# Kernel tuning notes

Hardware: AMD Instinct MI355X
Metric: run time of the kernel (lower is better)

## Reference

```python
import jax, jax.numpy as jnp
import numpy as np

B, D, OUT = 16384, 128, 32

def setup_inputs() -> dict:
    key = jax.random.key(0)
    kx, kw, kb = jax.random.split(key, 3)
    x = jax.random.normal(kx, (B, D), dtype=jnp.float32)
    # nn.Linear(in=D*(D+1), out=OUT): weight [OUT, D*(D+1)], bias [OUT]
    fan_in = D * (D + 1)
    bound = 1.0 / np.sqrt(fan_in)
    W = jax.random.uniform(kw, (OUT, fan_in), dtype=jnp.float32, minval=-bound, maxval=bound)
    b = jax.random.uniform(kb, (OUT,), dtype=jnp.float32, minval=-bound, maxval=bound)
    return {"x": x, "W": W, "b": b}

def reference(x, W, b):
    Bn, d = x.shape
    ones = jnp.ones((Bn, 1), dtype=x.dtype)
    xe = jnp.concatenate([x, ones], axis=-1)          # [B, d+1]
    # outer product z[b, i, j] = x[b, i] * xe[b, j]; flatten row-major -> [B, d*(d+1)]
    z = (x[:, :, None] * xe[:, None, :]).reshape(Bn, d * (d + 1))
    y = z @ W.T + b                                    # [B, OUT]
    return y
```

## Files before the change

kernel.cpp:

```cpp
#include <hip/hip_runtime.h>

typedef __attribute__((ext_vector_type(8)))  __bf16 bf16x8;
typedef __attribute__((ext_vector_type(16))) float  f32x16;
typedef unsigned int uint32;

#define D_IN  128
#define N_OUT 32
#define K129  129
#define WROW  16512
#define KE    144
#define NT    8
#define XQ_ELEMS (16384 * 128)
#define WQ_ELEMS (32 * 128 * KE)

__host__ __device__ __forceinline__ int permSlot(int s) {
    int q = s >> 3, h = (s >> 2) & 1, j = s & 3;
    return 16 * (q >> 1) + 8 * h + 4 * (q & 1) + j;
}

__global__ void prep(const float* __restrict__ x, const float* __restrict__ W,
                     __bf16* __restrict__ xq, __bf16* __restrict__ Wq) {
    int t = blockIdx.x * 256 + threadIdx.x;
    {
        const float4* s = reinterpret_cast<const float4*>(x) + (size_t)t * 2;
        float4 a = s[0], b = s[1];
        bf16x8 v = { (__bf16)a.x, (__bf16)a.y, (__bf16)a.z, (__bf16)a.w,
                     (__bf16)b.x, (__bf16)b.y, (__bf16)b.z, (__bf16)b.w };
        reinterpret_cast<bf16x8*>(xq)[t] = v;
    }
    for (int e = t; e < WQ_ELEMS; e += 262144) {
        int oi = e / KE, k = e - oi * KE;
        int o = oi >> 7, sg = oi & 127;
        int i = (sg & ~31) + permSlot(sg & 31);
        float v = (k <= D_IN) ? W[o * WROW + i * K129 + k] : 0.f;
        Wq[e] = (__bf16)v;
    }
}

#define STAGE(BUF, T)                                                              \
  do {                                                                             \
    if (PREP) {                                                                    \
      __builtin_amdgcn_global_load_lds(                                            \
        (const __attribute__((address_space(1))) uint32*)                          \
          (xq + ((rbase + (long)(T) * 32 + r0s) * D_IN + c0s * 8)),                \
        (__attribute__((address_space(3))) uint32*)(&tile[BUF][wave * 1024]),      \
        16, 0, 0);                                                                 \
      __builtin_amdgcn_global_load_lds(                                            \
        (const __attribute__((address_space(1))) uint32*)                          \
          (xq + ((rbase + (long)(T) * 32 + r1s) * D_IN + c1s * 8)),                \
        (__attribute__((address_space(3))) uint32*)(&tile[BUF][wave * 1024 + 512]),\
        16, 0, 0);                                                                 \
    } else {                                                                       \
      const float* s0 = x + (rbase + (long)(T) * 32 + r0s) * D_IN + c0s * 8;       \
      const float* s1 = x + (rbase + (long)(T) * 32 + r1s) * D_IN + c1s * 8;       \
      float4 a0 = *(const float4*)s0, a1 = *(const float4*)(s0 + 4);               \
      float4 b0 = *(const float4*)s1, b1 = *(const float4*)(s1 + 4);               \
      bf16x8 v0 = { (__bf16)a0.x,(__bf16)a0.y,(__bf16)a0.z,(__bf16)a0.w,           \
                    (__bf16)a1.x,(__bf16)a1.y,(__bf16)a1.z,(__bf16)a1.w };         \
      bf16x8 v1 = { (__bf16)b0.x,(__bf16)b0.y,(__bf16)b0.z,(__bf16)b0.w,           \
                    (__bf16)b1.x,(__bf16)b1.y,(__bf16)b1.z,(__bf16)b1.w };         \
      *(bf16x8*)&tile[BUF][(size_t)p0 * 8] = v0;                                   \
      *(bf16x8*)&tile[BUF][(size_t)p1 * 8] = v1;                                   \
    }                                                                              \
  } while (0)

#define COMPUTE(BUF, MT)                                                           \
  {                                                                                \
    const char* tb = (const char*)&tile[BUF][0];                                   \
    bf16x8 Bf[8];                                                                  \
    _Pragma("unroll")                                                              \
    for (int ks = 0; ks < 8; ++ks)                                                 \
      Bf[ks] = *reinterpret_cast<const bf16x8*>(tb + laneB[ks]);                   \
    float s = 0.f;                                                                 \
    _Pragma("unroll")                                                              \
    for (int ct = 0; ct < 4; ++ct) {                                               \
      f32x16 a;                                                                    \
      _Pragma("unroll")                                                            \
      for (int r = 0; r < 16; ++r) a[r] = 0.f;                                     \
      _Pragma("unroll")                                                            \
      for (int ks = 0; ks < 8; ++ks)                                               \
        a = __builtin_amdgcn_mfma_f32_32x32x16_bf16(A[ct][ks], Bf[ks], a, 0, 0, 0);\
      a = __builtin_amdgcn_mfma_f32_32x32x16_bf16(A[ct][8], B8c, a, 0, 0, 0);      \
      _Pragma("unroll")                                                            \
      for (int q = 0; q < 4; ++q)                                                  \
        _Pragma("unroll")                                                          \
        for (int j = 0; j < 4; ++j)                                                \
          s += a[q * 4 + j] * (float)Bf[2 * ct + (q >> 1)][4 * (q & 1) + j];       \
    }                                                                              \
    s += __shfl_xor(s, 32);                                                        \
    if (hi == 0)                                                                   \
      out[(rbase + (long)(MT) * 32 + b32) * N_OUT + o] = s + bias_o;               \
  }

template<int PREP>
__global__ __launch_bounds__(256, 2) void quad5(
    const float* __restrict__ x, const float* __restrict__ W,
    const __bf16* __restrict__ xq, const __bf16* __restrict__ Wq,
    const float* __restrict__ bias, float* __restrict__ out)
{
    __shared__ __align__(16) __bf16 tile[2][32 * 128];

    const int tid  = threadIdx.x;
    const int lane = tid & 63;
    const int wave = tid >> 6;
    const int b32  = lane & 31, hi = lane >> 5;

    const int bid = blockIdx.x;
    const int xcd = bid & 7, idx = bid >> 3;
    const int run = xcd * 8 + (idx & 7);
    const int og  = idx >> 3;
    const int o   = og * 4 + wave;
    const long rbase = (long)run * (NT * 32);
    const float bias_o = bias[o];

    bf16x8 A[4][9];
    #pragma unroll
    for (int ct = 0; ct < 4; ++ct) {
        if (PREP) {
            const __bf16* base = Wq + ((size_t)o * 128 + ct * 32 + b32) * KE + hi * 8;
            #pragma unroll
            for (int ks = 0; ks < 9; ++ks)
                A[ct][ks] = *reinterpret_cast<const bf16x8*>(base + ks * 16);
        } else {
            const int i = ct * 32 + permSlot(b32);
            const float* wr = W + (size_t)o * WROW + (size_t)i * K129;
            #pragma unroll
            for (int ks = 0; ks < 8; ++ks) {
                bf16x8 f;
                #pragma unroll
                for (int r = 0; r < 8; ++r) f[r] = (__bf16)wr[ks * 16 + hi * 8 + r];
                A[ct][ks] = f;
            }
            bf16x8 f;
            #pragma unroll
            for (int r = 0; r < 8; ++r) f[r] = (__bf16)0.f;
            if (hi == 0) f[0] = (__bf16)wr[128];
            A[ct][8] = f;
        }
    }

    bf16x8 B8c;
    #pragma unroll
    for (int r = 0; r < 8; ++r) B8c[r] = (__bf16)0.f;
    if (hi == 0) B8c[0] = (__bf16)1.0f;

    const int p0 = wave * 128 + lane;
    const int r0s = p0 >> 4, c0s = (p0 & 15) ^ (r0s & 15);
    const int p1 = p0 + 64;
    const int r1s = p1 >> 4, c1s = (p1 & 15) ^ (r1s & 15);

    const int rm = b32 & 15;
    int laneB[8];
    #pragma unroll
    for (int ks = 0; ks < 8; ++ks)
        laneB[ks] = b32 * 256 + (((ks * 2 + hi) ^ rm) << 4);

    STAGE(0, 0);
    __syncthreads();

    #pragma unroll
    for (int t2 = 0; t2 < NT / 2; ++t2) {
        if (t2 * 2 + 1 < NT) STAGE(1, t2 * 2 + 1);
        COMPUTE(0, t2 * 2);
        __syncthreads();
        if (t2 * 2 + 2 < NT) STAGE(0, t2 * 2 + 2);
        COMPUTE(1, t2 * 2 + 1);
        __syncthreads();
    }
}

extern "C" void kernel_launch(void* const* d_in, const int* in_sizes, int n_in,
                              void* d_out, int out_size, void* d_ws, size_t ws_size,
                              hipStream_t stream) {
    const float* x    = (const float*)d_in[0];
    const float* W    = (const float*)d_in[1];
    const float* bias = (const float*)d_in[2];
    float* out = (float*)d_out;

    const size_t need = (size_t)(XQ_ELEMS + WQ_ELEMS) * sizeof(__bf16);
    if (ws_size >= need) {
        __bf16* xq = (__bf16*)d_ws;
        __bf16* Wq = xq + XQ_ELEMS;
        prep<<<1024, 256, 0, stream>>>(x, W, xq, Wq);
        quad5<1><<<512, 256, 0, stream>>>(x, W, xq, Wq, bias, out);
    } else {
        quad5<0><<<512, 256, 0, stream>>>(x, W, (const __bf16*)nullptr,
                                          (const __bf16*)nullptr, bias, out);
    }
}
```

Baseline: 27.79 us.

## Deepen x-tile pipeline to four LDS buffers with vmcnt waits and deferred stores

Replaces the double-buffered LDS tile loop with a four-buffer ring that prefetches three tiles ahead. Each step waits only on the outstanding global-to-LDS loads it needs (explicit s_waitcnt vmcnt) and then issues a single s_barrier, instead of a full __syncthreads. It also raises wave priority around the MFMA block and holds the per-tile results in registers, writing all outputs at the end. The aim is to hide more load latency and cut synchronisation stalls, at the cost of double the LDS per block, which could lower occupancy. The hand-written vmcnt counts are only correct for the PREP path's async loads; in the non-PREP path a single barrier after synchronous LDS stores may be unsafe.

```diff
diff --git a/kernel.cpp b/kernel.cpp
--- a/kernel.cpp
+++ b/kernel.cpp
@@ -72,6 +72,7 @@
     for (int ks = 0; ks < 8; ++ks)                                                 \
       Bf[ks] = *reinterpret_cast<const bf16x8*>(tb + laneB[ks]);                   \
     float s = 0.f;                                                                 \
+    __builtin_amdgcn_s_setprio(1);                                                 \
     _Pragma("unroll")                                                              \
     for (int ct = 0; ct < 4; ++ct) {                                               \
       f32x16 a;                                                                    \
@@ -87,18 +88,29 @@
         for (int j = 0; j < 4; ++j)                                                \
           s += a[q * 4 + j] * (float)Bf[2 * ct + (q >> 1)][4 * (q & 1) + j];       \
     }                                                                              \
+    __builtin_amdgcn_s_setprio(0);                                                 \
     s += __shfl_xor(s, 32);                                                        \
-    if (hi == 0)                                                                   \
-      out[(rbase + (long)(MT) * 32 + b32) * N_OUT + o] = s + bias_o;               \
+    sArr[MT] = s;                                                                  \
   }
 
+#define WAITV(N) asm volatile("s_waitcnt vmcnt(" #N ")" ::: "memory")
+
+#define ITER(T, VN)                                                                \
+  {                                                                                \
+    WAITV(VN);                                                                     \
+    __builtin_amdgcn_s_barrier();                                                  \
+    asm volatile("" ::: "memory");                                                 \
+    if ((T) + 3 < NT) STAGE(((T) + 3) & 3, (T) + 3);                               \
+    COMPUTE((T) & 3, (T));                                                         \
+  }
+
 template<int PREP>
-__global__ __launch_bounds__(256, 2) void quad5(
+__global__ __launch_bounds__(256, 2) void quad6(
     const float* __restrict__ x, const float* __restrict__ W,
     const __bf16* __restrict__ xq, const __bf16* __restrict__ Wq,
     const float* __restrict__ bias, float* __restrict__ out)
 {
-    __shared__ __align__(16) __bf16 tile[2][32 * 128];
+    __shared__ __align__(16) __bf16 tile[4][32 * 128];
 
     const int tid  = threadIdx.x;
     const int lane = tid & 63;
@@ -155,17 +167,19 @@
     for (int ks = 0; ks < 8; ++ks)
         laneB[ks] = b32 * 256 + (((ks * 2 + hi) ^ rm) << 4);
 
+    float sArr[NT];
+
     STAGE(0, 0);
-    __syncthreads();
-
-    #pragma unroll
-    for (int t2 = 0; t2 < NT / 2; ++t2) {
-        if (t2 * 2 + 1 < NT) STAGE(1, t2 * 2 + 1);
-        COMPUTE(0, t2 * 2);
-        __syncthreads();
-        if (t2 * 2 + 2 < NT) STAGE(0, t2 * 2 + 2);
-        COMPUTE(1, t2 * 2 + 1);
-        __syncthreads();
+    STAGE(1, 1);
+    STAGE(2, 2);
+
+    ITER(0, 4); ITER(1, 4); ITER(2, 4); ITER(3, 4);
+    ITER(4, 4); ITER(5, 4); ITER(6, 2); ITER(7, 0);
+
+    if (hi == 0) {
+        #pragma unroll
+        for (int mt = 0; mt < NT; ++mt)
+            out[(rbase + (long)mt * 32 + b32) * N_OUT + o] = sArr[mt] + bias_o;
     }
 }
 
@@ -182,9 +196,9 @@
         __bf16* xq = (__bf16*)d_ws;
         __bf16* Wq = xq + XQ_ELEMS;
         prep<<<1024, 256, 0, stream>>>(x, W, xq, Wq);
-        quad5<1><<<512, 256, 0, stream>>>(x, W, xq, Wq, bias, out);
+        quad6<1><<<512, 256, 0, stream>>>(x, W, xq, Wq, bias, out);
     } else {
-        quad5<0><<<512, 256, 0, stream>>>(x, W, (const __bf16*)nullptr,
+        quad6<0><<<512, 256, 0, stream>>>(x, W, (const __bf16*)nullptr,
                                           (const __bf16*)nullptr, bias, out);
     }
 }
```

Result: slower. 40.59 us (+46.1%).

## Drop prep kernel and register-prefetch fp32 x two tiles ahead

Applied to the files above, without the earlier changes.

Removes the separate bf16 conversion kernel and its workspace, so the main kernel reads fp32 x and W directly and converts in registers. x tiles are loaded into registers two tiles ahead and written to the LDS double buffer after each compute step. Each step now ends with one lgkmcnt wait plus barrier instead of two __syncthreads. This saves a kernel launch and the extra round trip through the workspace, at the cost of more global bytes per tile, more registers, and per-thread strided W loads with conversion in every block.

```diff
diff --git a/kernel.cpp b/kernel.cpp
--- a/kernel.cpp
+++ b/kernel.cpp
@@ -2,66 +2,40 @@
 
 typedef __attribute__((ext_vector_type(8)))  __bf16 bf16x8;
 typedef __attribute__((ext_vector_type(16))) float  f32x16;
-typedef unsigned int uint32;
 
 #define D_IN  128
 #define N_OUT 32
 #define K129  129
 #define WROW  16512
-#define KE    144
 #define NT    8
-#define XQ_ELEMS (16384 * 128)
-#define WQ_ELEMS (32 * 128 * KE)
 
-__host__ __device__ __forceinline__ int permSlot(int s) {
+__device__ __forceinline__ int permSlot(int s) {
     int q = s >> 3, h = (s >> 2) & 1, j = s & 3;
     return 16 * (q >> 1) + 8 * h + 4 * (q & 1) + j;
 }
 
-__global__ void prep(const float* __restrict__ x, const float* __restrict__ W,
-                     __bf16* __restrict__ xq, __bf16* __restrict__ Wq) {
-    int t = blockIdx.x * 256 + threadIdx.x;
-    {
-        const float4* s = reinterpret_cast<const float4*>(x) + (size_t)t * 2;
-        float4 a = s[0], b = s[1];
-        bf16x8 v = { (__bf16)a.x, (__bf16)a.y, (__bf16)a.z, (__bf16)a.w,
-                     (__bf16)b.x, (__bf16)b.y, (__bf16)b.z, (__bf16)b.w };
-        reinterpret_cast<bf16x8*>(xq)[t] = v;
-    }
-    for (int e = t; e < WQ_ELEMS; e += 262144) {
-        int oi = e / KE, k = e - oi * KE;
-        int o = oi >> 7, sg = oi & 127;
-        int i = (sg & ~31) + permSlot(sg & 31);
-        float v = (k <= D_IN) ? W[o * WROW + i * K129 + k] : 0.f;
-        Wq[e] = (__bf16)v;
-    }
-}
+#define LOADR(T)                                                                   \
+  do {                                                                             \
+    const float* s0 = x + (rbase + (long)(T) * 32 + r0s) * D_IN + c0s * 8;         \
+    const float* s1 = x + (rbase + (long)(T) * 32 + r1s) * D_IN + c1s * 8;         \
+    g0a = *(const float4*)s0; g0b = *(const float4*)(s0 + 4);                      \
+    g1a = *(const float4*)s1; g1b = *(const float4*)(s1 + 4);                      \
+  } while (0)
 
-#define STAGE(BUF, T)                                                              \
+#define WRITES(BUF)                                                                \
   do {                                                                             \
-    if (PREP) {                                                                    \
-      __builtin_amdgcn_global_load_lds(                                            \
-        (const __attribute__((address_space(1))) uint32*)                          \
-          (xq + ((rbase + (long)(T) * 32 + r0s) * D_IN + c0s * 8)),                \
-        (__attribute__((address_space(3))) uint32*)(&tile[BUF][wave * 1024]),      \
-        16, 0, 0);                                                                 \
-      __builtin_amdgcn_global_load_lds(                                            \
-        (const __attribute__((address_space(1))) uint32*)                          \
-          (xq + ((rbase + (long)(T) * 32 + r1s) * D_IN + c1s * 8)),                \
-        (__attribute__((address_space(3))) uint32*)(&tile[BUF][wave * 1024 + 512]),\
-        16, 0, 0);                                                                 \
-    } else {                                                                       \
-      const float* s0 = x + (rbase + (long)(T) * 32 + r0s) * D_IN + c0s * 8;       \
-      const float* s1 = x + (rbase + (long)(T) * 32 + r1s) * D_IN + c1s * 8;       \
-      float4 a0 = *(const float4*)s0, a1 = *(const float4*)(s0 + 4);               \
-      float4 b0 = *(const float4*)s1, b1 = *(const float4*)(s1 + 4);               \
-      bf16x8 v0 = { (__bf16)a0.x,(__bf16)a0.y,(__bf16)a0.z,(__bf16)a0.w,           \
-                    (__bf16)a1.x,(__bf16)a1.y,(__bf16)a1.z,(__bf16)a1.w };         \
-      bf16x8 v1 = { (__bf16)b0.x,(__bf16)b0.y,(__bf16)b0.z,(__bf16)b0.w,           \
-                    (__bf16)b1.x,(__bf16)b1.y,(__bf16)b1.z,(__bf16)b1.w };         \
-      *(bf16x8*)&tile[BUF][(size_t)p0 * 8] = v0;                                   \
-      *(bf16x8*)&tile[BUF][(size_t)p1 * 8] = v1;                                   \
-    }                                                                              \
+    bf16x8 v0 = { (__bf16)g0a.x,(__bf16)g0a.y,(__bf16)g0a.z,(__bf16)g0a.w,         \
+                  (__bf16)g0b.x,(__bf16)g0b.y,(__bf16)g0b.z,(__bf16)g0b.w };       \
+    bf16x8 v1 = { (__bf16)g1a.x,(__bf16)g1a.y,(__bf16)g1a.z,(__bf16)g1a.w,         \
+                  (__bf16)g1b.x,(__bf16)g1b.y,(__bf16)g1b.z,(__bf16)g1b.w };       \
+    *(bf16x8*)&tile[BUF][(size_t)p0 * 8] = v0;                                     \
+    *(bf16x8*)&tile[BUF][(size_t)p1 * 8] = v1;                                     \
+  } while (0)
+
+#define BARRIER()                                                                  \
+  do {                                                                             \
+    asm volatile("s_waitcnt lgkmcnt(0)" ::: "memory");                             \
+    __builtin_amdgcn_s_barrier();                                                  \
   } while (0)
 
 #define COMPUTE(BUF, MT)                                                           \
@@ -92,10 +66,16 @@
       out[(rbase + (long)(MT) * 32 + b32) * N_OUT + o] = s + bias_o;               \
   }
 
-template<int PREP>
-__global__ __launch_bounds__(256, 2) void quad5(
+#define ITERF(T)                                                                   \
+  {                                                                                \
+    BARRIER();                                                                     \
+    COMPUTE((T) & 1, (T));                                                         \
+    if ((T) < NT - 1) { WRITES(((T) + 1) & 1); }                                   \
+    if ((T) < NT - 2) { LOADR((T) + 2); }                                          \
+  }
+
+__global__ __launch_bounds__(256, 2) void quad12(
     const float* __restrict__ x, const float* __restrict__ W,
-    const __bf16* __restrict__ xq, const __bf16* __restrict__ Wq,
     const float* __restrict__ bias, float* __restrict__ out)
 {
     __shared__ __align__(16) __bf16 tile[2][32 * 128];
@@ -116,27 +96,20 @@
     bf16x8 A[4][9];
     #pragma unroll
     for (int ct = 0; ct < 4; ++ct) {
-        if (PREP) {
-            const __bf16* base = Wq + ((size_t)o * 128 + ct * 32 + b32) * KE + hi * 8;
-            #pragma unroll
-            for (int ks = 0; ks < 9; ++ks)
-                A[ct][ks] = *reinterpret_cast<const bf16x8*>(base + ks * 16);
-        } else {
-            const int i = ct * 32 + permSlot(b32);
-            const float* wr = W + (size_t)o * WROW + (size_t)i * K129;
-            #pragma unroll
-            for (int ks = 0; ks < 8; ++ks) {
-                bf16x8 f;
-                #pragma unroll
-                for (int r = 0; r < 8; ++r) f[r] = (__bf16)wr[ks * 16 + hi * 8 + r];
-                A[ct][ks] = f;
-            }
+        const int i = ct * 32 + permSlot(b32);
+        const float* wr = W + (size_t)o * WROW + (size_t)i * K129;
+        #pragma unroll
+        for (int ks = 0; ks < 8; ++ks) {
             bf16x8 f;
             #pragma unroll
-            for (int r = 0; r < 8; ++r) f[r] = (__bf16)0.f;
-            if (hi == 0) f[0] = (__bf16)wr[128];
-            A[ct][8] = f;
+            for (int r = 0; r < 8; ++r) f[r] = (__bf16)wr[ks * 16 + hi * 8 + r];
+            A[ct][ks] = f;
         }
+        bf16x8 f;
+        #pragma unroll
+        for (int r = 0; r < 8; ++r) f[r] = (__bf16)0.f;
+        if (hi == 0) f[0] = (__bf16)wr[128];
+        A[ct][8] = f;
     }
 
     bf16x8 B8c;
@@ -155,18 +128,14 @@
     for (int ks = 0; ks < 8; ++ks)
         laneB[ks] = b32 * 256 + (((ks * 2 + hi) ^ rm) << 4);
 
-    STAGE(0, 0);
-    __syncthreads();
+    float4 g0a, g0b, g1a, g1b;
 
-    #pragma unroll
-    for (int t2 = 0; t2 < NT / 2; ++t2) {
-        if (t2 * 2 + 1 < NT) STAGE(1, t2 * 2 + 1);
-        COMPUTE(0, t2 * 2);
-        __syncthreads();
-        if (t2 * 2 + 2 < NT) STAGE(0, t2 * 2 + 2);
-        COMPUTE(1, t2 * 2 + 1);
-        __syncthreads();
-    }
+    LOADR(0);
+    WRITES(0);
+    LOADR(1);
+
+    ITERF(0); ITERF(1); ITERF(2); ITERF(3);
+    ITERF(4); ITERF(5); ITERF(6); ITERF(7);
 }
 
 extern "C" void kernel_launch(void* const* d_in, const int* in_sizes, int n_in,
@@ -177,14 +146,5 @@
     const float* bias = (const float*)d_in[2];
     float* out = (float*)d_out;
 
-    const size_t need = (size_t)(XQ_ELEMS + WQ_ELEMS) * sizeof(__bf16);
-    if (ws_size >= need) {
-        __bf16* xq = (__bf16*)d_ws;
-        __bf16* Wq = xq + XQ_ELEMS;
-        prep<<<1024, 256, 0, stream>>>(x, W, xq, Wq);
-        quad5<1><<<512, 256, 0, stream>>>(x, W, xq, Wq, bias, out);
-    } else {
-        quad5<0><<<512, 256, 0, stream>>>(x, W, (const __bf16*)nullptr,
-                                          (const __bf16*)nullptr, bias, out);
-    }
+    quad12<<<512, 256, 0, stream>>>(x, W, bias, out);
 }
```

Result: slower. 40.15 us (+44.5%).
